# Performance work log

Measured on AMD Instinct MI355X. Metric: run time of the kernel, lower is better.

The kernel has to match this reference:

```python
import jax, jax.numpy as jnp
import numpy as np

B, N, D = 32, 1024, 256
NHID = 512
NHID_HALF = NHID // 2
NCLASS = 2


def _xavier(key, shape):
    fan_in, fan_out = shape
    lim = float(np.sqrt(6.0 / (fan_in + fan_out)))
    return jax.random.uniform(key, shape, jnp.float32, -lim, lim)


def setup_inputs() -> dict:
    key = jax.random.key(0)
    ks = jax.random.split(key, 10)
    x = jax.random.normal(ks[0], (B, N, D), jnp.float32)
    adj = jax.random.uniform(ks[1], (B, N, N), jnp.float32)
    adj = adj / jnp.sum(adj, axis=-1, keepdims=True)  # row-normalized (mean aggregation)
    # GraphConv weights: shape (2*in_dim, out_dim) due to concat([x, agg(x)])
    W1 = _xavier(ks[2], (2 * D, NHID))
    b1 = jnp.zeros((NHID,), jnp.float32)
    W2 = _xavier(ks[3], (2 * NHID, NHID))
    b2 = jnp.zeros((NHID,), jnp.float32)
    W3 = _xavier(ks[4], (2 * NHID, NHID_HALF))
    b3 = jnp.zeros((NHID_HALF,), jnp.float32)
    W4 = _xavier(ks[5], (2 * NHID_HALF, NHID_HALF))
    b4 = jnp.zeros((NHID_HALF,), jnp.float32)
    # classifier: Linear(256,256) + PReLU(256) + Linear(256,2)
    cW1 = _xavier(ks[6], (NHID_HALF, NHID_HALF))
    cb1 = jnp.zeros((NHID_HALF,), jnp.float32)
    alpha = jnp.full((NHID_HALF,), 0.25, jnp.float32)
    cW2 = _xavier(ks[7], (NHID_HALF, NCLASS))
    cb2 = jnp.zeros((NCLASS,), jnp.float32)
    return {"x": x, "adj": adj, "W1": W1, "b1": b1, "W2": W2, "b2": b2,
            "W3": W3, "b3": b3, "W4": W4, "b4": b4,
            "cW1": cW1, "cb1": cb1, "alpha": alpha, "cW2": cW2, "cb2": cb2}


def _graphconv(x, adj, W, b):
    agg = jnp.einsum('bnm,bmd->bnd', adj, x)          # mean aggregation (adj row-normalized)
    cat = jnp.concatenate([x, agg], axis=-1)          # [B, N, 2*d]
    return jax.nn.relu(jnp.einsum('bnd,df->bnf', cat, W) + b)


def reference(x, adj, W1, b1, W2, b2, W3, b3, W4, b4, cW1, cb1, alpha, cW2, cb2):
    h = _graphconv(x, adj, W1, b1)
    h = _graphconv(h, adj, W2, b2)
    h = _graphconv(h, adj, W3, b3)
    h = _graphconv(h, adj, W4, b4)
    # classifier MLP with channel-wise PReLU
    h = jnp.einsum('bnd,df->bnf', h, cW1) + cb1
    h = jnp.where(h > 0, h, alpha * h)
    pred = jnp.einsum('bnd,df->bnf', h, cW2) + cb2
    return pred
```

## Files before the change

kernel.cpp:

```cpp
#include <hip/hip_runtime.h>

typedef short v8s __attribute__((ext_vector_type(8)));
typedef _Float16 v8h __attribute__((ext_vector_type(8)));
typedef float v4f __attribute__((ext_vector_type(4)));

#define BMT 128
#define BNT 128
#define BKT 32

__device__ __forceinline__ unsigned short f2bf(float f) {
    unsigned int u = __float_as_uint(f);
    u += 0x7fff + ((u >> 16) & 1);
    return (unsigned short)(u >> 16);
}
__device__ __forceinline__ unsigned short f2h(float f) {
    union { _Float16 h; unsigned short u; } c;
    c.h = (_Float16)f;
    return c.u;
}
__device__ __forceinline__ float h2f(unsigned short v) {
    union { unsigned short u; _Float16 h; } c;
    c.u = v;
    return (float)c.h;
}
__device__ __forceinline__ v8h as_h(v8s x) {
    union { v8s s; v8h h; } c;
    c.s = x;
    return c.h;
}

union U128 { unsigned short s[8]; uint4 v; };

__device__ __forceinline__ void gld16(const unsigned short* g, unsigned short* l) {
    __builtin_amdgcn_global_load_lds((const __attribute__((address_space(1))) void*)g,
                                     (__attribute__((address_space(3))) void*)l, 16, 0, 0);
}

__global__ __launch_bounds__(256) void split_hi(const float* __restrict__ x,
                                                unsigned short* __restrict__ oh, int n4) {
    int i = blockIdx.x * 256 + threadIdx.x;
    if (i < n4) {
        float4 f = ((const float4*)x)[i];
        float fv[4] = {f.x, f.y, f.z, f.w};
        ushort4 h;
        unsigned short* hp = (unsigned short*)&h;
#pragma unroll
        for (int j = 0; j < 4; ++j) hp[j] = f2bf(fv[j]);
        ((ushort4*)oh)[i] = h;
    }
}

__global__ __launch_bounds__(256) void tsplit16(const float* __restrict__ W,
                                                unsigned short* __restrict__ th, int R, int C) {
    __shared__ unsigned short lds[64][80];
    const int t = threadIdx.x;
    const int rt = blockIdx.x, ct = blockIdx.y;
    const int r = t >> 2, c0 = (t & 3) * 16;
    const float* src = W + (size_t)(rt * 64 + r) * C + ct * 64 + c0;
#pragma unroll
    for (int j = 0; j < 16; j += 4) {
        float4 f = *(const float4*)(src + j);
        lds[c0 + j + 0][r] = f2h(f.x);
        lds[c0 + j + 1][r] = f2h(f.y);
        lds[c0 + j + 2][r] = f2h(f.z);
        lds[c0 + j + 3][r] = f2h(f.w);
    }
    __syncthreads();
    const int c = t >> 2, r0 = (t & 3) * 16;
    U128 u0, u1;
#pragma unroll
    for (int j = 0; j < 8; ++j) { u0.s[j] = lds[c][r0 + j]; u1.s[j] = lds[c][r0 + 8 + j]; }
    unsigned short* dst = th + (size_t)(ct * 64 + c) * R + rt * 64 + r0;
    *(uint4*)dst = u0.v;
    *(uint4*)(dst + 8) = u1.v;
}

__global__ __launch_bounds__(256) void xprep(const float* __restrict__ src,
                                             unsigned short* __restrict__ th,
                                             unsigned short* __restrict__ x16, int d) {
    __shared__ unsigned int lds[64 * 66];
    const int t = threadIdx.x;
    const int mt = blockIdx.x, ft = blockIdx.y, z = blockIdx.z;
    const int r = t >> 3, c8 = (t & 7) * 8;
#pragma unroll
    for (int half = 0; half < 2; ++half) {
        int rr = r + half * 32;
        size_t grow = (size_t)z * 1024 + mt * 64 + rr;
        const float* xs = src + grow * d + ft * 64 + c8;
        float4 f0 = *(const float4*)xs;
        float4 f1 = *(const float4*)(xs + 4);
        float fv[8] = {f0.x, f0.y, f0.z, f0.w, f1.x, f1.y, f1.z, f1.w};
        U128 uh;
#pragma unroll
        for (int j = 0; j < 8; ++j) {
            lds[rr * 66 + c8 + j] = f2bf(fv[j]);
            uh.s[j] = f2h(fv[j]);
        }
        *(uint4*)(x16 + grow * d + ft * 64 + c8) = uh.v;
    }
    __syncthreads();
    const int f = t >> 3, m0 = (t & 7) * 8;
#pragma unroll
    for (int half = 0; half < 2; ++half) {
        int ff = f + half * 32;
        U128 uh;
#pragma unroll
        for (int j = 0; j < 8; ++j)
            uh.s[j] = (unsigned short)lds[(m0 + j) * 66 + ff];
        size_t orow = ((size_t)z * d + ft * 64 + ff) * 1024 + mt * 64 + m0;
        *(uint4*)(th + orow) = uh.v;
    }
}

template <int ACT, bool TWO, int AMODE, int DT, bool WRT>
__global__ __launch_bounds__(256) void gemm128(
    const void* a1, const unsigned short* __restrict__ a2,
    int K1, int K2,
    const unsigned short* __restrict__ b_, int ldb,
    const float* __restrict__ bias, const float* __restrict__ alpha,
    unsigned short* __restrict__ o_, int Nout,
    unsigned short* __restrict__ th,
    size_t aZ, size_t bZ, int cZRows,
    int nblk, int mBits)
{
    constexpr int LA = (AMODE == 0) ? 32 : 40;
    constexpr int LB = 32;
    __shared__ __align__(16) unsigned short Ash[BMT * LA];
    __shared__ __align__(16) unsigned short Bsh[BNT * LB];

    const int t = threadIdx.x;
    const int lane = t & 63, wave = t >> 6;
    const int wm = wave >> 1, wn = wave & 1;
    const int l15 = lane & 15, quad = lane >> 4;

    const int bx = blockIdx.x;
    const int low3 = bx & 7, rest = bx >> 3;
    const int nIdx = rest % nblk, g = rest / nblk;
    const int grp = g * 8 + low3;
    const int m0 = (grp & ((1 << mBits) - 1)) * BMT;
    const int zb = grp >> mBits;
    const int n0 = nIdx * BNT;

    const unsigned short* bhz = b_ + (size_t)zb * bZ;

    v4f acc[4][4] = {};

    const int nch = TWO ? 2 : 1;
    for (int ch = 0; ch < nch; ++ch) {
        const int K = (TWO && ch) ? K2 : K1;
        const int kr0 = (TWO && ch) ? K1 : 0;
        const unsigned short* ah = nullptr;
        const float* af = nullptr;
        if constexpr (AMODE == 0)
            ah = (ch ? a2 : (const unsigned short*)a1) + (size_t)zb * aZ;
        else
            af = (const float*)a1 + (size_t)zb * aZ;

        for (int kk = 0; kk < K; kk += BKT) {
            __syncthreads();
            if constexpr (AMODE == 0) {
#pragma unroll
                for (int i = 0; i < 2; ++i) {
                    int s = i * 256 + t;
                    int row = s >> 2;
                    int cg = (s & 3) ^ ((s >> 3) & 3);
                    size_t go = (size_t)(m0 + row) * K + kk + cg * 8;
                    int ls = (i * 256 + (t & ~63)) * 8;
                    gld16(ah + go, &Ash[ls]);
                }
            } else {
#pragma unroll
                for (int i = 0; i < 2; ++i) {
                    int cid = i * 256 + t;
                    int row = cid >> 2, c = cid & 3;
                    const float* src = af + (size_t)(m0 + row) * K + kk + c * 8;
                    float4 f0 = *(const float4*)src;
                    float4 f1 = *(const float4*)(src + 4);
                    float fv[8] = {f0.x, f0.y, f0.z, f0.w, f1.x, f1.y, f1.z, f1.w};
                    U128 uh;
#pragma unroll
                    for (int j = 0; j < 8; ++j) uh.s[j] = f2bf(fv[j]);
                    *(uint4*)&Ash[row * LA + c * 8] = uh.v;
                }
            }
#pragma unroll
            for (int i = 0; i < 2; ++i) {
                int s = i * 256 + t;
                int row = s >> 2;
                int cg = (s & 3) ^ ((s >> 3) & 3);
                size_t go = (size_t)(n0 + row) * ldb + kr0 + kk + cg * 8;
                int ls = (i * 256 + (t & ~63)) * 8;
                gld16(bhz + go, &Bsh[ls]);
            }
            __syncthreads();
            v8s ahf[4];
#pragma unroll
            for (int mi = 0; mi < 4; ++mi) {
                int row = wm * 64 + mi * 16 + l15;
                int off;
                if constexpr (AMODE == 0) off = row * LA + ((quad ^ ((row >> 1) & 3)) * 8);
                else                      off = row * LA + quad * 8;
                ahf[mi] = *(const v8s*)&Ash[off];
            }
#pragma unroll
            for (int ni = 0; ni < 4; ++ni) {
                int row = wn * 64 + ni * 16 + l15;
                int off = row * LB + ((quad ^ ((row >> 1) & 3)) * 8);
                v8s bhf = *(const v8s*)&Bsh[off];
#pragma unroll
                for (int mi = 0; mi < 4; ++mi) {
                    if constexpr (DT == 0)
                        acc[mi][ni] = __builtin_amdgcn_mfma_f32_16x16x32_bf16(ahf[mi], bhf, acc[mi][ni], 0, 0, 0);
                    else
                        acc[mi][ni] = __builtin_amdgcn_mfma_f32_16x16x32_f16(as_h(ahf[mi]), as_h(bhf), acc[mi][ni], 0, 0, 0);
                }
            }
        }
    }

    const size_t crow0 = (size_t)zb * cZRows + m0;
#pragma unroll
    for (int ni = 0; ni < 4; ++ni) {
        int n = n0 + wn * 64 + ni * 16 + l15;
        float bv = (ACT > 0) ? bias[n] : 0.f;
        float av = (ACT == 2) ? alpha[n] : 0.f;
#pragma unroll
        for (int mi = 0; mi < 4; ++mi) {
#pragma unroll
            for (int r = 0; r < 4; ++r) {
                int m = wm * 64 + mi * 16 + quad * 4 + r;
                float v = acc[mi][ni][r] + bv;
                if (ACT == 1) v = v > 0.f ? v : 0.f;
                if (ACT == 2) v = v > 0.f ? v : av * v;
                acc[mi][ni][r] = v;
                o_[(crow0 + m) * (size_t)Nout + n] = f2h(v);
            }
        }
    }

    if constexpr (WRT) {
        const int zbT = m0 >> 10;
        const int mloc0 = (m0 & 1023) + wm * 64;
#pragma unroll
        for (int ni = 0; ni < 4; ++ni) {
            int f = n0 + wn * 64 + ni * 16 + l15;
            size_t rowb = (((size_t)zbT * Nout + f) << 10) + mloc0;
#pragma unroll
            for (int mi = 0; mi < 4; ++mi) {
                ushort4 u;
                unsigned short* up = (unsigned short*)&u;
#pragma unroll
                for (int r = 0; r < 4; ++r) up[r] = f2bf(acc[mi][ni][r]);
                *(ushort4*)(th + rowb + mi * 16 + quad * 4) = u;
            }
        }
    }
}

template <int ACT, bool TWO, int DT, bool WRT, int BN2, bool Z32>
__global__ __launch_bounds__(512, 2) void gemm256(
    const unsigned short* __restrict__ a1, const unsigned short* __restrict__ a2,
    int K1, int K2,
    const unsigned short* __restrict__ b_, int ldb,
    const float* __restrict__ bias, const float* __restrict__ alpha,
    unsigned short* __restrict__ o_, int Nout,
    unsigned short* __restrict__ th,
    size_t aZ, size_t bZ, int cZRows)
{
    constexpr int ASLOT = 256 * 32;
    constexpr int BSLOT = BN2 * 32;
    constexpr int SLOT  = ASLOT + BSLOT;
    constexpr int LPT   = 2 + BN2 / 128;
    constexpr int WN    = BN2 / 64;
    constexpr int WM    = 8 / WN;
    constexpr int MREP  = 16 / WM;
    constexpr int NPH   = MREP / 2;
    __shared__ __align__(16) unsigned short lds[4 * SLOT];

    const int t = threadIdx.x;
    const int lane = t & 63, wave = t >> 6;
    const int wm = wave / WN, wn = wave % WN;
    const int l15 = lane & 15, quad = lane >> 4;

    const int bx = blockIdx.x;
    const int xcd = bx & 7, loc = bx >> 3;
    int zb, mIdx, nIdx;
    if constexpr (Z32) {
        zb = xcd * 4 + (loc >> 3);
        mIdx = (loc >> 1) & 3;
        nIdx = loc & 1;
    } else {
        zb = 0;
        mIdx = xcd * 16 + (loc >> 1);
        nIdx = loc & 1;
    }
    const int m0 = mIdx * 256;
    const int n0 = nIdx * BN2;

    const unsigned short* A1 = a1 + (size_t)zb * aZ;
    const unsigned short* A2p = TWO ? (a2 + (size_t)zb * aZ) : nullptr;
    const unsigned short* B = b_ + (size_t)zb * bZ;

    const int NT1 = K1 >> 5;
    const int NTtot = NT1 + (TWO ? (K2 >> 5) : 0);

    auto stage_part = [&](int tt, int p) {
        unsigned short* slot = &lds[(tt & 3) * SLOT];
        const unsigned short* abase;
        int astr;
        if constexpr (TWO) {
            if (tt >= NT1) { abase = A2p + ((size_t)(tt - NT1) << 5); astr = K2; }
            else           { abase = A1 + ((size_t)tt << 5); astr = K1; }
        } else {
            abase = A1 + ((size_t)tt << 5); astr = K1;
        }
        auto lda = [&](int i) {
            int s = i * 512 + t;
            int row = s >> 2;
            int cg = (s & 3) ^ ((s >> 3) & 3);
            gld16(abase + (size_t)(m0 + row) * astr + cg * 8,
                  &slot[(i * 512 + (t & ~63)) * 8]);
        };
        auto ldb_ = [&](int i) {
            const unsigned short* bbase = B + ((size_t)tt << 5);
            int s = i * 512 + t;
            int row = s >> 2;
            int cg = (s & 3) ^ ((s >> 3) & 3);
            gld16(bbase + (size_t)(n0 + row) * ldb + cg * 8,
                  &slot[ASLOT + (i * 512 + (t & ~63)) * 8]);
        };
        if constexpr (BN2 == 256) {
            if (p < 2) lda(p); else ldb_(p - 2);
        } else {
            if (p == 0) { lda(0); lda(1); } else ldb_(0);
        }
    };
    auto stage_all = [&](int tt) {
#pragma unroll
        for (int p = 0; p < NPH; ++p) stage_part(tt, p);
    };

    v4f acc[MREP][4] = {};

    auto rdA = [&](const unsigned short* slot, int mi) -> v8s {
        int row = wm * (MREP * 16) + mi * 16 + l15;
        return *(const v8s*)&slot[row * 32 + ((quad ^ ((row >> 1) & 3)) * 8)];
    };
    auto rdB = [&](const unsigned short* slot, int ni) -> v8s {
        int row = wn * 64 + ni * 16 + l15;
        return *(const v8s*)&slot[ASLOT + row * 32 + ((quad ^ ((row >> 1) & 3)) * 8)];
    };

    auto wait_lpt = [&]() {
        if constexpr (LPT == 4) asm volatile("s_waitcnt vmcnt(4)" ::: "memory");
        else                    asm volatile("s_waitcnt vmcnt(3)" ::: "memory");
    };

    stage_all(0); stage_all(1); stage_all(2);
    wait_lpt();
    __builtin_amdgcn_s_barrier();
    asm volatile("" ::: "memory");

    for (int tt = 0; tt < NTtot; ++tt) {
        const unsigned short* slot = &lds[(tt & 3) * SLOT];
        const bool st = (tt + 3 < NTtot);
        v8s bf[4];
#pragma unroll
        for (int q = 0; q < NPH; ++q) {
            if (q == 0) {
#pragma unroll
                for (int ni = 0; ni < 4; ++ni) bf[ni] = rdB(slot, ni);
            }
            v8s a0 = rdA(slot, 2 * q);
            v8s a1 = rdA(slot, 2 * q + 1);
            if (st) stage_part(tt + 3, q);
            __builtin_amdgcn_s_barrier();
            asm volatile("" ::: "memory");
            __builtin_amdgcn_s_setprio(1);
#pragma unroll
            for (int ni = 0; ni < 4; ++ni) {
                if constexpr (DT == 0) {
                    acc[2 * q][ni]     = __builtin_amdgcn_mfma_f32_16x16x32_bf16(a0, bf[ni], acc[2 * q][ni], 0, 0, 0);
                    acc[2 * q + 1][ni] = __builtin_amdgcn_mfma_f32_16x16x32_bf16(a1, bf[ni], acc[2 * q + 1][ni], 0, 0, 0);
                } else {
                    acc[2 * q][ni]     = __builtin_amdgcn_mfma_f32_16x16x32_f16(as_h(a0), as_h(bf[ni]), acc[2 * q][ni], 0, 0, 0);
                    acc[2 * q + 1][ni] = __builtin_amdgcn_mfma_f32_16x16x32_f16(as_h(a1), as_h(bf[ni]), acc[2 * q + 1][ni], 0, 0, 0);
                }
            }
            __builtin_amdgcn_s_setprio(0);
        }
        if (tt + 2 < NTtot) {
            if (tt + 3 < NTtot) wait_lpt();
            else                asm volatile("s_waitcnt vmcnt(0)" ::: "memory");
            __builtin_amdgcn_s_barrier();
            asm volatile("" ::: "memory");
        }
    }

    const size_t crow0 = (size_t)zb * cZRows + m0;
#pragma unroll
    for (int ni = 0; ni < 4; ++ni) {
        int n = n0 + wn * 64 + ni * 16 + l15;
        float bv = (ACT > 0) ? bias[n] : 0.f;
        float av = (ACT == 2) ? alpha[n] : 0.f;
#pragma unroll
        for (int mi = 0; mi < MREP; ++mi) {
#pragma unroll
            for (int r = 0; r < 4; ++r) {
                int m = wm * (MREP * 16) + mi * 16 + quad * 4 + r;
                float v = acc[mi][ni][r] + bv;
                if (ACT == 1) v = v > 0.f ? v : 0.f;
                if (ACT == 2) v = v > 0.f ? v : av * v;
                acc[mi][ni][r] = v;
                o_[(crow0 + m) * (size_t)Nout + n] = f2h(v);
            }
        }
    }

    if constexpr (WRT) {
        const int zbT = m0 >> 10;
        const int mloc0 = (m0 & 1023) + wm * (MREP * 16);
#pragma unroll
        for (int ni = 0; ni < 4; ++ni) {
            int f = n0 + wn * 64 + ni * 16 + l15;
            size_t rowb = (((size_t)zbT * Nout + f) << 10) + mloc0;
#pragma unroll
            for (int mi = 0; mi < MREP; ++mi) {
                ushort4 u;
                unsigned short* up = (unsigned short*)&u;
#pragma unroll
                for (int r = 0; r < 4; ++r) up[r] = f2bf(acc[mi][ni][r]);
                *(ushort4*)(th + rowb + mi * 16 + quad * 4) = u;
            }
        }
    }
}

__global__ __launch_bounds__(256) void final_gemm(const unsigned short* __restrict__ hh,
                                                  const float* __restrict__ W,
                                                  const float* __restrict__ bias,
                                                  float* __restrict__ out) {
    const int t = threadIdx.x;
    const int m = blockIdx.x * 64 + (t >> 2);
    const int kq = (t & 3) * 64;
    const unsigned short* ph = hh + (size_t)m * 256 + kq;
    float a0 = 0.f, a1 = 0.f;
#pragma unroll
    for (int i = 0; i < 8; ++i) {
        uint4 vh = *(const uint4*)(ph + i * 8);
        const unsigned short* sh = (const unsigned short*)&vh;
#pragma unroll
        for (int j = 0; j < 8; ++j) {
            int k = kq + i * 8 + j;
            float h = h2f(sh[j]);
            a0 += h * W[k * 2];
            a1 += h * W[k * 2 + 1];
        }
    }
    a0 += __shfl_down(a0, 2); a0 += __shfl_down(a0, 1);
    a1 += __shfl_down(a1, 2); a1 += __shfl_down(a1, 1);
    if ((t & 3) == 0) {
        out[(size_t)m * 2] = a0 + bias[0];
        out[(size_t)m * 2 + 1] = a1 + bias[1];
    }
}

extern "C" void kernel_launch(void* const* d_in, const int* in_sizes, int n_in,
                              void* d_out, int out_size, void* d_ws, size_t ws_size,
                              hipStream_t stream) {
    const float* x   = (const float*)d_in[0];
    const float* adj = (const float*)d_in[1];
    const float* W1  = (const float*)d_in[2];
    const float* b1  = (const float*)d_in[3];
    const float* W2  = (const float*)d_in[4];
    const float* b2  = (const float*)d_in[5];
    const float* W3  = (const float*)d_in[6];
    const float* b3  = (const float*)d_in[7];
    const float* W4  = (const float*)d_in[8];
    const float* b4  = (const float*)d_in[9];
    const float* cW1 = (const float*)d_in[10];
    const float* cb1 = (const float*)d_in[11];
    const float* alp = (const float*)d_in[12];
    const float* cW2 = (const float*)d_in[13];
    const float* cb2 = (const float*)d_in[14];
    float* out = (float*)d_out;

    const size_t P   = 32768ull * 512;
    const size_t XP  = 32768ull * 256;
    const size_t WT_TOT = 1245184;
    const size_t ADJ = 32ull * 1024 * 1024;

    unsigned short* N1  = (unsigned short*)d_ws;
    unsigned short* N2  = N1 + P;
    unsigned short* N3  = N2 + P;
    unsigned short* Th  = N3 + P;
    unsigned short* X16 = Th + P;
    unsigned short* WT  = X16 + XP;
    unsigned short* SA  = WT + WT_TOT;

    const size_t o1 = 0, o2 = 262144, o3 = 786432, o4 = 1048576, o5 = 1179648;
    const bool preAdj = ws_size >= (4 * P + XP + WT_TOT + ADJ) * sizeof(unsigned short);

    dim3 blk(256);
    dim3 blk5(512);

    tsplit16<<<dim3(8, 8),  blk, 0, stream>>>(W1,  WT + o1, 512, 512);
    tsplit16<<<dim3(16, 8), blk, 0, stream>>>(W2,  WT + o2, 1024, 512);
    tsplit16<<<dim3(16, 4), blk, 0, stream>>>(W3,  WT + o3, 1024, 256);
    tsplit16<<<dim3(8, 4),  blk, 0, stream>>>(W4,  WT + o4, 512, 256);
    tsplit16<<<dim3(4, 4),  blk, 0, stream>>>(cW1, WT + o5, 256, 256);
    if (preAdj)
        split_hi<<<32768, blk, 0, stream>>>(adj, SA, (int)(ADJ / 4));

    xprep<<<dim3(16, 4, 32), blk, 0, stream>>>(x, Th, X16, 256);

    if (preAdj)
        gemm256<0, false, 0, false, 128, true><<<256, blk5, 0, stream>>>(
            SA, nullptr, 1024, 0, Th, 1024, nullptr, nullptr,
            N2, 256, nullptr, (size_t)1 << 20, 256ull * 1024, 1024);
    else
        gemm128<0, false, 1, 0, false><<<512, blk, 0, stream>>>(
            adj, nullptr, 1024, 0, Th, 1024, nullptr, nullptr,
            N2, 256, nullptr, (size_t)1 << 20, 256ull * 1024, 1024, 2, 3);

    gemm256<1, true, 1, true, 256, false><<<256, blk5, 0, stream>>>(
        X16, N2, 256, 256, WT + o1, 512, b1, nullptr,
        N3, 512, Th, 0, 0, 0);

    if (preAdj)
        gemm256<0, false, 0, false, 256, true><<<256, blk5, 0, stream>>>(
            SA, nullptr, 1024, 0, Th, 1024, nullptr, nullptr,
            N1, 512, nullptr, (size_t)1 << 20, 512ull * 1024, 1024);
    else
        gemm128<0, false, 1, 0, false><<<1024, blk, 0, stream>>>(
            adj, nullptr, 1024, 0, Th, 1024, nullptr, nullptr,
            N1, 512, nullptr, (size_t)1 << 20, 512ull * 1024, 1024, 4, 3);

    gemm256<1, true, 1, true, 256, false><<<256, blk5, 0, stream>>>(
        N3, N1, 512, 512, WT + o2, 1024, b2, nullptr,
        N2, 512, Th, 0, 0, 0);

    if (preAdj)
        gemm256<0, false, 0, false, 256, true><<<256, blk5, 0, stream>>>(
            SA, nullptr, 1024, 0, Th, 1024, nullptr, nullptr,
            N1, 512, nullptr, (size_t)1 << 20, 512ull * 1024, 1024);
    else
        gemm128<0, false, 1, 0, false><<<1024, blk, 0, stream>>>(
            adj, nullptr, 1024, 0, Th, 1024, nullptr, nullptr,
            N1, 512, nullptr, (size_t)1 << 20, 512ull * 1024, 1024, 4, 3);

    gemm256<1, true, 1, true, 128, false><<<256, blk5, 0, stream>>>(
        N2, N1, 512, 512, WT + o3, 1024, b3, nullptr,
        N3, 256, Th, 0, 0, 0);

    if (preAdj)
        gemm256<0, false, 0, false, 128, true><<<256, blk5, 0, stream>>>(
            SA, nullptr, 1024, 0, Th, 1024, nullptr, nullptr,
            N1, 256, nullptr, (size_t)1 << 20, 256ull * 1024, 1024);
    else
        gemm128<0, false, 1, 0, false><<<512, blk, 0, stream>>>(
            adj, nullptr, 1024, 0, Th, 1024, nullptr, nullptr,
            N1, 256, nullptr, (size_t)1 << 20, 256ull * 1024, 1024, 2, 3);

    gemm256<1, true, 1, false, 128, false><<<256, blk5, 0, stream>>>(
        N3, N1, 256, 256, WT + o4, 512, b4, nullptr,
        N2, 256, nullptr, 0, 0, 0);

    gemm256<2, false, 1, false, 128, false><<<256, blk5, 0, stream>>>(
        N2, nullptr, 256, 0, WT + o5, 256, cb1, alp,
        N3, 256, nullptr, 0, 0, 0);

    final_gemm<<<512, blk, 0, stream>>>(N3, cW2, cb2, out);
}
```

Measured before the change: 540.1 us.

## Shrink GEMM tiles to 128 wide, triple-buffer LDS, double grid size

```diff
diff --git a/kernel.cpp b/kernel.cpp
--- a/kernel.cpp
+++ b/kernel.cpp
@@ -257,8 +257,8 @@
     }
 }
 
-template <int ACT, bool TWO, int DT, bool WRT, int BN2, bool Z32>
-__global__ __launch_bounds__(512, 2) void gemm256(
+template <int ACT, bool TWO, int DT, bool WRT, int BM, int BN2, int NB, bool Z32>
+__global__ __launch_bounds__(512, 4) void gemm256(
     const unsigned short* __restrict__ a1, const unsigned short* __restrict__ a2,
     int K1, int K2,
     const unsigned short* __restrict__ b_, int ldb,
@@ -267,15 +267,18 @@
     unsigned short* __restrict__ th,
     size_t aZ, size_t bZ, int cZRows)
 {
-    constexpr int ASLOT = 256 * 32;
+    constexpr int ASLOT = BM * 32;
     constexpr int BSLOT = BN2 * 32;
     constexpr int SLOT  = ASLOT + BSLOT;
-    constexpr int LPT   = 2 + BN2 / 128;
+    constexpr int AR    = BM / 128;
+    constexpr int BR    = BN2 / 128;
+    constexpr int LPT   = AR + BR;
     constexpr int WN    = BN2 / 64;
     constexpr int WM    = 8 / WN;
-    constexpr int MREP  = 16 / WM;
-    constexpr int NPH   = MREP / 2;
-    __shared__ __align__(16) unsigned short lds[4 * SLOT];
+    constexpr int MREP  = BM / (WM * 16);
+    constexpr int NPH   = (MREP >= 2) ? MREP / 2 : 1;
+    constexpr int NSH   = (NB == 4) ? 2 : 1;
+    __shared__ __align__(16) unsigned short lds[3 * SLOT];
 
     const int t = threadIdx.x;
     const int lane = t & 63, wave = t >> 6;
@@ -286,15 +289,17 @@
     const int xcd = bx & 7, loc = bx >> 3;
     int zb, mIdx, nIdx;
     if constexpr (Z32) {
-        zb = xcd * 4 + (loc >> 3);
-        mIdx = (loc >> 1) & 3;
-        nIdx = loc & 1;
+        zb = xcd * 4 + (loc >> 4);
+        int l = loc & 15;
+        mIdx = l >> NSH;
+        nIdx = l & (NB - 1);
     } else {
+        constexpr int MC = 32768 / BM;
         zb = 0;
-        mIdx = xcd * 16 + (loc >> 1);
-        nIdx = loc & 1;
-    }
-    const int m0 = mIdx * 256;
+        mIdx = xcd * (MC / 8) + (loc >> NSH);
+        nIdx = loc & (NB - 1);
+    }
+    const int m0 = mIdx * BM + (Z32 ? 0 : 0);
     const int n0 = nIdx * BN2;
 
     const unsigned short* A1 = a1 + (size_t)zb * aZ;
@@ -304,8 +309,7 @@
     const int NT1 = K1 >> 5;
     const int NTtot = NT1 + (TWO ? (K2 >> 5) : 0);
 
-    auto stage_part = [&](int tt, int p) {
-        unsigned short* slot = &lds[(tt & 3) * SLOT];
+    auto stage_part = [&](unsigned short* slot, int tt, int p) {
         const unsigned short* abase;
         int astr;
         if constexpr (TWO) {
@@ -321,7 +325,7 @@
             gld16(abase + (size_t)(m0 + row) * astr + cg * 8,
                   &slot[(i * 512 + (t & ~63)) * 8]);
         };
-        auto ldb_ = [&](int i) {
+        auto ldbf = [&](int i) {
             const unsigned short* bbase = B + ((size_t)tt << 5);
             int s = i * 512 + t;
             int row = s >> 2;
@@ -329,15 +333,19 @@
             gld16(bbase + (size_t)(n0 + row) * ldb + cg * 8,
                   &slot[ASLOT + (i * 512 + (t & ~63)) * 8]);
         };
-        if constexpr (BN2 == 256) {
-            if (p < 2) lda(p); else ldb_(p - 2);
+        if constexpr (NPH == 1) {
+#pragma unroll
+            for (int i = 0; i < AR; ++i) lda(i);
+#pragma unroll
+            for (int i = 0; i < BR; ++i) ldbf(i);
         } else {
-            if (p == 0) { lda(0); lda(1); } else ldb_(0);
+            if (p == 0) { lda(0); lda(1); }
+            else        { ldbf(0); }
         }
     };
-    auto stage_all = [&](int tt) {
-#pragma unroll
-        for (int p = 0; p < NPH; ++p) stage_part(tt, p);
+    auto stage_all = [&](unsigned short* slot, int tt) {
+#pragma unroll
+        for (int p = 0; p < NPH; ++p) stage_part(slot, tt, p);
     };
 
     v4f acc[MREP][4] = {};
@@ -352,18 +360,23 @@
     };
 
     auto wait_lpt = [&]() {
-        if constexpr (LPT == 4) asm volatile("s_waitcnt vmcnt(4)" ::: "memory");
-        else                    asm volatile("s_waitcnt vmcnt(3)" ::: "memory");
+        if constexpr (LPT == 4)      asm volatile("s_waitcnt vmcnt(4)" ::: "memory");
+        else if constexpr (LPT == 3) asm volatile("s_waitcnt vmcnt(3)" ::: "memory");
+        else                         asm volatile("s_waitcnt vmcnt(2)" ::: "memory");
     };
 
-    stage_all(0); stage_all(1); stage_all(2);
+    stage_all(&lds[0], 0);
+    stage_all(&lds[SLOT], 1);
     wait_lpt();
     __builtin_amdgcn_s_barrier();
     asm volatile("" ::: "memory");
 
+    int cs = 0;
     for (int tt = 0; tt < NTtot; ++tt) {
-        const unsigned short* slot = &lds[(tt & 3) * SLOT];
-        const bool st = (tt + 3 < NTtot);
+        unsigned short* slot = &lds[cs * SLOT];
+        int ssIdx = cs + 2; if (ssIdx >= 3) ssIdx -= 3;
+        unsigned short* sslot = &lds[ssIdx * SLOT];
+        const bool st = (tt + 2 < NTtot);
         v8s bf[4];
 #pragma unroll
         for (int q = 0; q < NPH; ++q) {
@@ -371,30 +384,33 @@
 #pragma unroll
                 for (int ni = 0; ni < 4; ++ni) bf[ni] = rdB(slot, ni);
             }
-            v8s a0 = rdA(slot, 2 * q);
-            v8s a1 = rdA(slot, 2 * q + 1);
-            if (st) stage_part(tt + 3, q);
+            v8s a0, a1;
+            if constexpr (NPH == 1) { a0 = rdA(slot, 0); a1 = rdA(slot, 1); }
+            else                    { a0 = rdA(slot, 2 * q); a1 = rdA(slot, 2 * q + 1); }
+            if (st) stage_part(sslot, tt + 2, q);
             __builtin_amdgcn_s_barrier();
             asm volatile("" ::: "memory");
             __builtin_amdgcn_s_setprio(1);
+            const int mb = (NPH == 1) ? 0 : 2 * q;
 #pragma unroll
             for (int ni = 0; ni < 4; ++ni) {
                 if constexpr (DT == 0) {
-                    acc[2 * q][ni]     = __builtin_amdgcn_mfma_f32_16x16x32_bf16(a0, bf[ni], acc[2 * q][ni], 0, 0, 0);
-                    acc[2 * q + 1][ni] = __builtin_amdgcn_mfma_f32_16x16x32_bf16(a1, bf[ni], acc[2 * q + 1][ni], 0, 0, 0);
+                    acc[mb][ni]     = __builtin_amdgcn_mfma_f32_16x16x32_bf16(a0, bf[ni], acc[mb][ni], 0, 0, 0);
+                    acc[mb + 1][ni] = __builtin_amdgcn_mfma_f32_16x16x32_bf16(a1, bf[ni], acc[mb + 1][ni], 0, 0, 0);
                 } else {
-                    acc[2 * q][ni]     = __builtin_amdgcn_mfma_f32_16x16x32_f16(as_h(a0), as_h(bf[ni]), acc[2 * q][ni], 0, 0, 0);
-                    acc[2 * q + 1][ni] = __builtin_amdgcn_mfma_f32_16x16x32_f16(as_h(a1), as_h(bf[ni]), acc[2 * q + 1][ni], 0, 0, 0);
+                    acc[mb][ni]     = __builtin_amdgcn_mfma_f32_16x16x32_f16(as_h(a0), as_h(bf[ni]), acc[mb][ni], 0, 0, 0);
+                    acc[mb + 1][ni] = __builtin_amdgcn_mfma_f32_16x16x32_f16(as_h(a1), as_h(bf[ni]), acc[mb + 1][ni], 0, 0, 0);
                 }
             }
             __builtin_amdgcn_s_setprio(0);
         }
-        if (tt + 2 < NTtot) {
-            if (tt + 3 < NTtot) wait_lpt();
-            else                asm volatile("s_waitcnt vmcnt(0)" ::: "memory");
+        if (tt + 1 < NTtot) {
+            if (st) wait_lpt();
+            else    asm volatile("s_waitcnt vmcnt(0)" ::: "memory");
             __builtin_amdgcn_s_barrier();
             asm volatile("" ::: "memory");
         }
+        cs = (cs == 2) ? 0 : cs + 1;
     }
 
     const size_t crow0 = (size_t)zb * cZRows + m0;
@@ -515,7 +531,7 @@
     xprep<<<dim3(16, 4, 32), blk, 0, stream>>>(x, Th, X16, 256);
 
     if (preAdj)
-        gemm256<0, false, 0, false, 128, true><<<256, blk5, 0, stream>>>(
+        gemm256<0, false, 0, false, 128, 128, 2, true><<<512, blk5, 0, stream>>>(
             SA, nullptr, 1024, 0, Th, 1024, nullptr, nullptr,
             N2, 256, nullptr, (size_t)1 << 20, 256ull * 1024, 1024);
     else
@@ -523,12 +539,12 @@
             adj, nullptr, 1024, 0, Th, 1024, nullptr, nullptr,
             N2, 256, nullptr, (size_t)1 << 20, 256ull * 1024, 1024, 2, 3);
 
-    gemm256<1, true, 1, true, 256, false><<<256, blk5, 0, stream>>>(
+    gemm256<1, true, 1, true, 256, 128, 4, false><<<512, blk5, 0, stream>>>(
         X16, N2, 256, 256, WT + o1, 512, b1, nullptr,
         N3, 512, Th, 0, 0, 0);
 
     if (preAdj)
-        gemm256<0, false, 0, false, 256, true><<<256, blk5, 0, stream>>>(
+        gemm256<0, false, 0, false, 256, 128, 4, true><<<512, blk5, 0, stream>>>(
             SA, nullptr, 1024, 0, Th, 1024, nullptr, nullptr,
             N1, 512, nullptr, (size_t)1 << 20, 512ull * 1024, 1024);
     else
@@ -536,12 +552,12 @@
             adj, nullptr, 1024, 0, Th, 1024, nullptr, nullptr,
             N1, 512, nullptr, (size_t)1 << 20, 512ull * 1024, 1024, 4, 3);
 
-    gemm256<1, true, 1, true, 256, false><<<256, blk5, 0, stream>>>(
+    gemm256<1, true, 1, true, 256, 128, 4, false><<<512, blk5, 0, stream>>>(
         N3, N1, 512, 512, WT + o2, 1024, b2, nullptr,
         N2, 512, Th, 0, 0, 0);
 
     if (preAdj)
-        gemm256<0, false, 0, false, 256, true><<<256, blk5, 0, stream>>>(
+        gemm256<0, false, 0, false, 256, 128, 4, true><<<512, blk5, 0, stream>>>(
             SA, nullptr, 1024, 0, Th, 1024, nullptr, nullptr,
             N1, 512, nullptr, (size_t)1 << 20, 512ull * 1024, 1024);
     else
@@ -549,12 +565,12 @@
             adj, nullptr, 1024, 0, Th, 1024, nullptr, nullptr,
             N1, 512, nullptr, (size_t)1 << 20, 512ull * 1024, 1024, 4, 3);
 
-    gemm256<1, true, 1, true, 128, false><<<256, blk5, 0, stream>>>(
+    gemm256<1, true, 1, true, 128, 128, 2, false><<<512, blk5, 0, stream>>>(
         N2, N1, 512, 512, WT + o3, 1024, b3, nullptr,
         N3, 256, Th, 0, 0, 0);
 
     if (preAdj)
-        gemm256<0, false, 0, false, 128, true><<<256, blk5, 0, stream>>>(
+        gemm256<0, false, 0, false, 128, 128, 2, true><<<512, blk5, 0, stream>>>(
             SA, nullptr, 1024, 0, Th, 1024, nullptr, nullptr,
             N1, 256, nullptr, (size_t)1 << 20, 256ull * 1024, 1024);
     else
@@ -562,11 +578,11 @@
             adj, nullptr, 1024, 0, Th, 1024, nullptr, nullptr,
             N1, 256, nullptr, (size_t)1 << 20, 256ull * 1024, 1024, 2, 3);
 
-    gemm256<1, true, 1, false, 128, false><<<256, blk5, 0, stream>>>(
+    gemm256<1, true, 1, false, 128, 128, 2, false><<<512, blk5, 0, stream>>>(
         N3, N1, 256, 256, WT + o4, 512, b4, nullptr,
         N2, 256, nullptr, 0, 0, 0);
 
-    gemm256<2, false, 1, false, 128, false><<<256, blk5, 0, stream>>>(
+    gemm256<2, false, 1, false, 128, 128, 2, false><<<512, blk5, 0, stream>>>(
         N2, nullptr, 256, 0, WT + o5, 256, cb1, alp,
         N3, 256, nullptr, 0, 0, 0);
 
```

Result: no change. 530.5 us (-1.8%).
